# Kernel tuning notes

Measured on AMD Instinct MI355X. Metric: run time of the kernel, lower is better.

The kernel has to match this reference:

```python
import jax, jax.numpy as jnp
import numpy as np

NEG_INF = -1e9  # Keras uses a large negative for masked logits


def setup_inputs() -> dict:
    key = jax.random.key(0)
    k1, k2, k3, k4, k5 = jax.random.split(key, 5)
    B, Tq, Tv, D, U = 8, 128, 128, 512, 1024
    query = jax.random.normal(k1, (B, Tq, D), dtype=jnp.float32)
    value = jax.random.normal(k2, (B, Tv, D), dtype=jnp.float32)
    mask = jnp.ones((B, Tv), dtype=bool)
    # Dense(units, use_bias=False) kernels and AdditiveAttention scale vector
    W1 = jax.random.normal(k3, (D, U), dtype=jnp.float32) * (1.0 / np.sqrt(D))
    W2 = jax.random.normal(k4, (D, U), dtype=jnp.float32) * (1.0 / np.sqrt(D))
    scale = jax.random.normal(k5, (U,), dtype=jnp.float32) * (1.0 / np.sqrt(U))
    return {"query": query, "value": value, "mask": mask,
            "W1": W1, "W2": W2, "scale": scale}


def reference(query, value, mask, W1, W2, scale):
    # Projections (Dense, no bias)
    wq = jnp.einsum('btd,du->btu', query, W1)   # [B, Tq, U]
    wk = jnp.einsum('bsd,du->bsu', value, W2)   # [B, Tv, U]
    # Additive (Bahdanau) scores: sum_u scale_u * tanh(wq + wk)
    # Materializes [B, Tq, Tv, U] broadcast-add like Keras AdditiveAttention.
    scores = jnp.einsum('u,btsu->bts', scale,
                        jnp.tanh(wq[:, :, None, :] + wk[:, None, :, :]))
    # value mask over key axis (query_mask is all-ones in the source -> no-op)
    scores = jnp.where(mask[:, None, :], scores, NEG_INF)
    attn = jax.nn.softmax(scores, axis=-1)       # [B, Tq, Tv]
    context = jnp.einsum('bts,bsd->btd', attn, value)  # [B, Tq, D]
    return context, attn
```

## Files before the change

### kernel.cpp

```cpp
#include <hip/hip_runtime.h>

#define B_  8
#define TQ  128
#define TV  128
#define DIM 512
#define UU  1024
#define NSPLIT 8
#define NP  (B_ * TQ * TV)
#define C2  2.885390081777927f

typedef __attribute__((ext_vector_type(8))) short     short8;
typedef __attribute__((ext_vector_type(4))) float     f32x4;
typedef __attribute__((ext_vector_type(4))) unsigned short us4;

__device__ __forceinline__ unsigned short bf16_rtne(float x) {
    unsigned u = __float_as_uint(x);
    unsigned r = u + 0x7FFF + ((u >> 16) & 1);
    return (unsigned short)(r >> 16);
}
__device__ __forceinline__ float bf16_to_f(unsigned short h) {
    return __uint_as_float(((unsigned)h) << 16);
}

__global__ __launch_bounds__(256) void k_prep(
    const float* __restrict__ Q, const float* __restrict__ Vv,
    const float* __restrict__ W1, const float* __restrict__ W2,
    unsigned short* __restrict__ Ah, unsigned short* __restrict__ Al,
    unsigned short* __restrict__ Wh, unsigned short* __restrict__ Wl)
{
    __shared__ float ts[32][36];
    const int bx = blockIdx.x;
    const int t  = threadIdx.x;

    if (bx < 1024) {
        int idx = bx * 256 + t;
        int mat = idx >> 17;
        const float* src = mat ? Vv : Q;
        int off = (idx & 131071) * 4;
        float4 v = *(const float4*)&src[off];
        us4 h, l;
        h.x = bf16_rtne(v.x); l.x = bf16_rtne(v.x - bf16_to_f(h.x));
        h.y = bf16_rtne(v.y); l.y = bf16_rtne(v.y - bf16_to_f(h.y));
        h.z = bf16_rtne(v.z); l.z = bf16_rtne(v.z - bf16_to_f(h.z));
        h.w = bf16_rtne(v.w); l.w = bf16_rtne(v.w - bf16_to_f(h.w));
        *(us4*)&Ah[mat * 524288 + off] = h;
        *(us4*)&Al[mat * 524288 + off] = l;
    } else {
        int b2   = bx - 1024;
        int mat  = b2 >> 9;
        int tile = b2 & 511;
        int n0 = (tile & 31) * 32;
        int k0 = (tile >> 5) * 32;
        const float* W = mat ? W2 : W1;

        int kk = t >> 3, n4 = (t & 7) * 4;
        float4 w = *(const float4*)&W[(k0 + kk) * UU + n0 + n4];
        ts[n4 + 0][kk] = w.x; ts[n4 + 1][kk] = w.y;
        ts[n4 + 2][kk] = w.z; ts[n4 + 3][kk] = w.w;
        __syncthreads();

        int nn = t >> 3, k4 = (t & 7) * 4;
        float4 v = *(const float4*)&ts[nn][k4];
        us4 h, l;
        h.x = bf16_rtne(v.x); l.x = bf16_rtne(v.x - bf16_to_f(h.x));
        h.y = bf16_rtne(v.y); l.y = bf16_rtne(v.y - bf16_to_f(h.y));
        h.z = bf16_rtne(v.z); l.z = bf16_rtne(v.z - bf16_to_f(h.z));
        h.w = bf16_rtne(v.w); l.w = bf16_rtne(v.w - bf16_to_f(h.w));
        unsigned off = mat * 524288 + (n0 + nn) * 512 + k0 + k4;
        *(us4*)&Wh[off] = h;
        *(us4*)&Wl[off] = l;
    }
}

#define PKP 72
__global__ __launch_bounds__(256) void k_proj(
    const unsigned short* __restrict__ Ah, const unsigned short* __restrict__ Al,
    const unsigned short* __restrict__ Bh, const unsigned short* __restrict__ Bl,
    float* __restrict__ Eq, float* __restrict__ Ek)
{
    __shared__ short sAh[64 * PKP], sAl[64 * PKP], sBh[64 * PKP], sBl[64 * PKP];

    const int tid  = threadIdx.x;
    const int wave = tid >> 6;
    const int lane = tid & 63;
    const int mat  = blockIdx.z;
    const int m0   = blockIdx.y * 64;
    const int n0   = blockIdx.x * 64;

    const unsigned mb = mat * 524288u;
    const int wm = (wave & 1) * 32;
    const int wn = (wave >> 1) * 32;

    const int sm = tid >> 2, sg = tid & 3;
    const unsigned short* gAh = Ah + mb + (m0 + sm) * 512;
    const unsigned short* gAl = Al + mb + (m0 + sm) * 512;
    const unsigned short* gBh = Bh + mb + (n0 + sm) * 512;
    const unsigned short* gBl = Bl + mb + (n0 + sm) * 512;
    const int so0 = sm * PKP + sg * 8;
    const int so1 = sm * PKP + 32 + sg * 8;

    const int fr = lane & 15, fq = lane >> 4;
    const int aOff0 = (wm + fr) * PKP + fq * 8;
    const int aOff1 = (wm + 16 + fr) * PKP + fq * 8;
    const int bOff0 = (wn + fr) * PKP + fq * 8;
    const int bOff1 = (wn + 16 + fr) * PKP + fq * 8;

    f32x4 acc00 = {0.f, 0.f, 0.f, 0.f};
    f32x4 acc01 = {0.f, 0.f, 0.f, 0.f};
    f32x4 acc10 = {0.f, 0.f, 0.f, 0.f};
    f32x4 acc11 = {0.f, 0.f, 0.f, 0.f};

    int4 rAh0, rAh1, rAl0, rAl1, rBh0, rBh1, rBl0, rBl1;
    #define LOADALL(K)                                                       \
        rAh0 = *(const int4*)(gAh + (K) + sg * 8);                           \
        rAh1 = *(const int4*)(gAh + (K) + 32 + sg * 8);                      \
        rAl0 = *(const int4*)(gAl + (K) + sg * 8);                           \
        rAl1 = *(const int4*)(gAl + (K) + 32 + sg * 8);                      \
        rBh0 = *(const int4*)(gBh + (K) + sg * 8);                           \
        rBh1 = *(const int4*)(gBh + (K) + 32 + sg * 8);                      \
        rBl0 = *(const int4*)(gBl + (K) + sg * 8);                           \
        rBl1 = *(const int4*)(gBl + (K) + 32 + sg * 8);

    LOADALL(0)

    #pragma unroll 1
    for (int kc = 0; kc < 8; ++kc) {
        *(int4*)&sAh[so0] = rAh0;  *(int4*)&sAh[so1] = rAh1;
        *(int4*)&sAl[so0] = rAl0;  *(int4*)&sAl[so1] = rAl1;
        *(int4*)&sBh[so0] = rBh0;  *(int4*)&sBh[so1] = rBh1;
        *(int4*)&sBl[so0] = rBl0;  *(int4*)&sBl[so1] = rBl1;
        __syncthreads();

        if (kc < 7) { LOADALL((kc + 1) * 64) }

        #pragma unroll
        for (int ks = 0; ks < 2; ++ks) {
            const int o = ks * 32;
            short8 a0h = *(const short8*)&sAh[aOff0 + o];
            short8 a0l = *(const short8*)&sAl[aOff0 + o];
            short8 a1h = *(const short8*)&sAh[aOff1 + o];
            short8 a1l = *(const short8*)&sAl[aOff1 + o];
            short8 b0h = *(const short8*)&sBh[bOff0 + o];
            short8 b0l = *(const short8*)&sBl[bOff0 + o];
            short8 b1h = *(const short8*)&sBh[bOff1 + o];
            short8 b1l = *(const short8*)&sBl[bOff1 + o];

            acc00 = __builtin_amdgcn_mfma_f32_16x16x32_bf16(a0h, b0h, acc00, 0, 0, 0);
            acc00 = __builtin_amdgcn_mfma_f32_16x16x32_bf16(a0h, b0l, acc00, 0, 0, 0);
            acc00 = __builtin_amdgcn_mfma_f32_16x16x32_bf16(a0l, b0h, acc00, 0, 0, 0);

            acc01 = __builtin_amdgcn_mfma_f32_16x16x32_bf16(a0h, b1h, acc01, 0, 0, 0);
            acc01 = __builtin_amdgcn_mfma_f32_16x16x32_bf16(a0h, b1l, acc01, 0, 0, 0);
            acc01 = __builtin_amdgcn_mfma_f32_16x16x32_bf16(a0l, b1h, acc01, 0, 0, 0);

            acc10 = __builtin_amdgcn_mfma_f32_16x16x32_bf16(a1h, b0h, acc10, 0, 0, 0);
            acc10 = __builtin_amdgcn_mfma_f32_16x16x32_bf16(a1h, b0l, acc10, 0, 0, 0);
            acc10 = __builtin_amdgcn_mfma_f32_16x16x32_bf16(a1l, b0h, acc10, 0, 0, 0);

            acc11 = __builtin_amdgcn_mfma_f32_16x16x32_bf16(a1h, b1h, acc11, 0, 0, 0);
            acc11 = __builtin_amdgcn_mfma_f32_16x16x32_bf16(a1h, b1l, acc11, 0, 0, 0);
            acc11 = __builtin_amdgcn_mfma_f32_16x16x32_bf16(a1l, b1h, acc11, 0, 0, 0);
        }
        __syncthreads();
    }
    #undef LOADALL

    float* C = mat ? Ek : Eq;
    #pragma unroll
    for (int r = 0; r < 4; ++r) {
        int row0 = m0 + wm + fq * 4 + r;
        int row1 = row0 + 16;
        int col0 = n0 + wn + fr;
        C[row0 * UU + col0]      = __builtin_amdgcn_exp2f(C2 * acc00[r]);
        C[row0 * UU + col0 + 16] = __builtin_amdgcn_exp2f(C2 * acc01[r]);
        C[row1 * UU + col0]      = __builtin_amdgcn_exp2f(C2 * acc10[r]);
        C[row1 * UU + col0 + 16] = __builtin_amdgcn_exp2f(C2 * acc11[r]);
    }
}
#undef PKP

__global__ __launch_bounds__(256) void k_scores(
    const float* __restrict__ Eq, const float* __restrict__ Ek,
    const float* __restrict__ scale, float* __restrict__ part)
{
    __shared__ float qs[32][132];
    __shared__ float ks[32][132];
    __shared__ float ss[128];

    const int tid = threadIdx.x;
    const int tx  = tid & 15;
    const int ty  = tid >> 4;
    const int b   = blockIdx.z & 7;
    const int us  = blockIdx.z >> 3;
    const int t0  = blockIdx.y * 32;
    const int s0  = blockIdx.x * 32;
    const int u0  = us * (UU / NSPLIT);

    {
        const int c  = (tid & 31) * 4;
        const int r0 = tid >> 5;
        #pragma unroll
        for (int i = 0; i < 4; ++i) {
            int r = r0 + i * 8;
            *(float4*)&qs[r][c] = *(const float4*)&Eq[(b * TQ + t0 + r) * UU + u0 + c];
            *(float4*)&ks[r][c] = *(const float4*)&Ek[(b * TV + s0 + r) * UU + u0 + c];
        }
        if (tid < 32)
            *(float4*)&ss[tid * 4] = *(const float4*)&scale[u0 + tid * 4];
    }
    __syncthreads();

    float a00 = 0.f, a01 = 0.f, a10 = 0.f, a11 = 0.f;

    #pragma unroll 4
    for (int u4 = 0; u4 < 32; ++u4) {
        float4 q0 = *(const float4*)&qs[ty][u4 * 4];
        float4 q1 = *(const float4*)&qs[ty + 16][u4 * 4];
        float4 k0 = *(const float4*)&ks[tx][u4 * 4];
        float4 k1 = *(const float4*)&ks[tx + 16][u4 * 4];
        float4 sv = *(const float4*)&ss[u4 * 4];

        #define PAIR(ACC, QV, KV)                                           \
        {                                                                   \
            float p1 = QV.x * KV.x, p2 = QV.y * KV.y;                       \
            float b1 = p1 + 1.f,   b2 = p2 + 1.f;                           \
            float n1 = fmaf(sv.y, b1, sv.x * b2);                           \
            ACC = fmaf(n1, __builtin_amdgcn_rcpf(b1 * b2), ACC);            \
            float p3 = QV.z * KV.z, p4 = QV.w * KV.w;                       \
            float b3 = p3 + 1.f,   b4 = p4 + 1.f;                           \
            float n2 = fmaf(sv.w, b3, sv.z * b4);                           \
            ACC = fmaf(n2, __builtin_amdgcn_rcpf(b3 * b4), ACC);            \
        }
        PAIR(a00, q0, k0)
        PAIR(a01, q0, k1)
        PAIR(a10, q1, k0)
        PAIR(a11, q1, k1)
        #undef PAIR
    }

    const int t = t0 + ty, s = s0 + tx;
    float* p = &part[us * NP + (b * TQ + t) * TV + s];
    p[0]            = a00;
    p[16]           = a01;
    p[16 * TV]      = a10;
    p[16 * TV + 16] = a11;
}

__global__ __launch_bounds__(256) void k_ctx(
    const float* __restrict__ part, const int* __restrict__ mask,
    const float* __restrict__ Vv,
    float* __restrict__ attn, float* __restrict__ ctx)
{
    __shared__ float at[128][20];

    const int tid = threadIdx.x;
    const int dc  = blockIdx.x;
    const int tt  = blockIdx.y;
    const int b   = blockIdx.z;
    const int t0  = tt * 16;
    const int rg  = tid >> 4;
    const int ln  = tid & 15;
    const int base = (b * TQ + t0 + rg) * TV;

    float x[8];
    #pragma unroll
    for (int j = 0; j < 8; ++j) {
        const int s = ln + 16 * j;
        float p = 0.f;
        #pragma unroll
        for (int i = 0; i < NSPLIT; ++i) p += part[i * NP + base + s];
        x[j] = mask[b * TV + s] ? -2.f * p : -1e9f;
    }
    float m = x[0];
    #pragma unroll
    for (int j = 1; j < 8; ++j) m = fmaxf(m, x[j]);
    #pragma unroll
    for (int o = 8; o > 0; o >>= 1) m = fmaxf(m, __shfl_xor(m, o, 64));
    const float L2E = 1.4426950408889634f;
    float e[8];
    float sum = 0.f;
    #pragma unroll
    for (int j = 0; j < 8; ++j) {
        e[j] = __builtin_amdgcn_exp2f((x[j] - m) * L2E);
        sum += e[j];
    }
    #pragma unroll
    for (int o = 8; o > 0; o >>= 1) sum += __shfl_xor(sum, o, 64);
    const float r = __builtin_amdgcn_rcpf(sum);
    #pragma unroll
    for (int j = 0; j < 8; ++j) {
        const float a = e[j] * r;
        at[ln + 16 * j][rg] = a;
        if (dc == 0) attn[base + ln + 16 * j] = a;
    }
    __syncthreads();

    const int d  = (tid & 127) + dc * 128;
    const int tg = tid >> 7;
    float acc[8] = {};
    const float* vp = &Vv[b * TV * DIM + d];
    for (int s = 0; s < TV; ++s) {
        float v = vp[s * DIM];
        float4 a0 = *(const float4*)&at[s][tg * 8];
        float4 a1 = *(const float4*)&at[s][tg * 8 + 4];
        acc[0] = fmaf(a0.x, v, acc[0]);
        acc[1] = fmaf(a0.y, v, acc[1]);
        acc[2] = fmaf(a0.z, v, acc[2]);
        acc[3] = fmaf(a0.w, v, acc[3]);
        acc[4] = fmaf(a1.x, v, acc[4]);
        acc[5] = fmaf(a1.y, v, acc[5]);
        acc[6] = fmaf(a1.z, v, acc[6]);
        acc[7] = fmaf(a1.w, v, acc[7]);
    }
    #pragma unroll
    for (int j = 0; j < 8; ++j) {
        int t = t0 + tg * 8 + j;
        ctx[(b * TQ + t) * DIM + d] = acc[j];
    }
}

extern "C" void kernel_launch(void* const* d_in, const int* in_sizes, int n_in,
                              void* d_out, int out_size, void* d_ws, size_t ws_size,
                              hipStream_t stream)
{
    const float* query = (const float*)d_in[0];
    const float* value = (const float*)d_in[1];
    const int*   mask  = (const int*)d_in[2];
    const float* W1    = (const float*)d_in[3];
    const float* W2    = (const float*)d_in[4];
    const float* scale = (const float*)d_in[5];

    float* out  = (float*)d_out;
    float* ctx  = out;
    float* attn = out + B_ * TQ * DIM;

    float* Eq   = (float*)d_ws;
    float* Ek   = Eq + 1024 * 1024;
    float* part = Ek + 1024 * 1024;
    unsigned short* Ah = (unsigned short*)(part + NSPLIT * NP);
    unsigned short* Al = Ah + 2 * 1024 * 512;
    unsigned short* Wh = Al + 2 * 1024 * 512;
    unsigned short* Wl = Wh + 2 * 1024 * 512;

    hipLaunchKernelGGL(k_prep,   dim3(2048),            dim3(256), 0, stream,
                       query, value, W1, W2, Ah, Al, Wh, Wl);
    hipLaunchKernelGGL(k_proj,   dim3(16, 16, 2),       dim3(256), 0, stream,
                       Ah, Al, Wh, Wl, Eq, Ek);
    hipLaunchKernelGGL(k_scores, dim3(4, 4, 8 * NSPLIT), dim3(256), 0, stream,
                       Eq, Ek, scale, part);
    hipLaunchKernelGGL(k_ctx,    dim3(4, 8, 8),         dim3(256), 0, stream,
                       part, mask, value, attn, ctx);
}
```

Measured before the change: 112.9 us.

## Enlarge score tiles to 64x64 with 4x4 register blocking and XCD-swizzle projection blocks

The scores kernel now computes 64x64 (query, key) tiles per block with a 4x4 per-thread register tile. This cuts LDS loads per tanh-pair evaluation, and it permutes key rows in shared memory to avoid bank conflicts. The U split doubles to 16 to keep enough blocks in flight, which doubles the partial-sum buffer the context kernel must read and reduce. The projection GEMM is launched as a flat 1D grid with a block-index remap that spreads tiles across XCDs for better L2 locality.

```diff
diff --git a/kernel.cpp b/kernel.cpp
--- a/kernel.cpp
+++ b/kernel.cpp
@@ -5,7 +5,7 @@
 #define TV  128
 #define DIM 512
 #define UU  1024
-#define NSPLIT 8
+#define NSPLIT 16
 #define NP  (B_ * TQ * TV)
 #define C2  2.885390081777927f
 
@@ -83,9 +83,16 @@
     const int tid  = threadIdx.x;
     const int wave = tid >> 6;
     const int lane = tid & 63;
-    const int mat  = blockIdx.z;
-    const int m0   = blockIdx.y * 64;
-    const int n0   = blockIdx.x * 64;
+
+    const int flat = blockIdx.x;
+    const int x    = flat & 7;
+    const int j    = flat >> 3;
+    const int pair = x * 4 + (j >> 4);
+    const int nt   = pair & 15;
+    const int mat  = pair >> 4;
+    const int mt   = j & 15;
+    const int m0   = mt * 64;
+    const int n0   = nt * 64;
 
     const unsigned mb = mat * 524288u;
     const int wm = (wave & 1) * 32;
@@ -183,67 +190,69 @@
     const float* __restrict__ Eq, const float* __restrict__ Ek,
     const float* __restrict__ scale, float* __restrict__ part)
 {
-    __shared__ float qs[32][132];
-    __shared__ float ks[32][132];
-    __shared__ float ss[128];
+    __shared__ float qs[64][68];
+    __shared__ float ks[64][68];
+    __shared__ float ss[64];
 
     const int tid = threadIdx.x;
     const int tx  = tid & 15;
     const int ty  = tid >> 4;
     const int b   = blockIdx.z & 7;
     const int us  = blockIdx.z >> 3;
-    const int t0  = blockIdx.y * 32;
-    const int s0  = blockIdx.x * 32;
+    const int t0  = blockIdx.y * 64;
+    const int s0  = blockIdx.x * 64;
     const int u0  = us * (UU / NSPLIT);
 
     {
-        const int c  = (tid & 31) * 4;
-        const int r0 = tid >> 5;
+        const int r  = tid >> 2;
+        const int c0 = (tid & 3) * 16;
+        const float* srq = &Eq[(b * TQ + t0 + r) * UU + u0 + c0];
+        const float* srk = &Ek[(b * TV + s0 + r) * UU + u0 + c0];
+        const int rp = (r >> 2) | ((r & 3) << 4);
         #pragma unroll
         for (int i = 0; i < 4; ++i) {
-            int r = r0 + i * 8;
-            *(float4*)&qs[r][c] = *(const float4*)&Eq[(b * TQ + t0 + r) * UU + u0 + c];
-            *(float4*)&ks[r][c] = *(const float4*)&Ek[(b * TV + s0 + r) * UU + u0 + c];
+            *(float4*)&qs[r][c0 + i * 4]  = *(const float4*)(srq + i * 4);
+            *(float4*)&ks[rp][c0 + i * 4] = *(const float4*)(srk + i * 4);
         }
-        if (tid < 32)
+        if (tid < 16)
             *(float4*)&ss[tid * 4] = *(const float4*)&scale[u0 + tid * 4];
     }
     __syncthreads();
 
-    float a00 = 0.f, a01 = 0.f, a10 = 0.f, a11 = 0.f;
-
-    #pragma unroll 4
-    for (int u4 = 0; u4 < 32; ++u4) {
-        float4 q0 = *(const float4*)&qs[ty][u4 * 4];
-        float4 q1 = *(const float4*)&qs[ty + 16][u4 * 4];
-        float4 k0 = *(const float4*)&ks[tx][u4 * 4];
-        float4 k1 = *(const float4*)&ks[tx + 16][u4 * 4];
+    float acc[4][4] = {};
+
+    #pragma unroll 2
+    for (int u4 = 0; u4 < 16; ++u4) {
+        float4 q[4], k[4];
+        #pragma unroll
+        for (int i = 0; i < 4; ++i)
+            q[i] = *(const float4*)&qs[ty * 4 + i][u4 * 4];
+        #pragma unroll
+        for (int jj = 0; jj < 4; ++jj)
+            k[jj] = *(const float4*)&ks[tx + (jj << 4)][u4 * 4];
         float4 sv = *(const float4*)&ss[u4 * 4];
 
-        #define PAIR(ACC, QV, KV)                                           \
-        {                                                                   \
-            float p1 = QV.x * KV.x, p2 = QV.y * KV.y;                       \
-            float b1 = p1 + 1.f,   b2 = p2 + 1.f;                           \
-            float n1 = fmaf(sv.y, b1, sv.x * b2);                           \
-            ACC = fmaf(n1, __builtin_amdgcn_rcpf(b1 * b2), ACC);            \
-            float p3 = QV.z * KV.z, p4 = QV.w * KV.w;                       \
-            float b3 = p3 + 1.f,   b4 = p4 + 1.f;                           \
-            float n2 = fmaf(sv.w, b3, sv.z * b4);                           \
-            ACC = fmaf(n2, __builtin_amdgcn_rcpf(b3 * b4), ACC);            \
+        #pragma unroll
+        for (int i = 0; i < 4; ++i) {
+            #pragma unroll
+            for (int jj = 0; jj < 4; ++jj) {
+                float p1 = q[i].x * k[jj].x, p2 = q[i].y * k[jj].y;
+                float b1 = p1 + 1.f,        b2 = p2 + 1.f;
+                float n1 = fmaf(sv.y, b1, sv.x * b2);
+                acc[i][jj] = fmaf(n1, __builtin_amdgcn_rcpf(b1 * b2), acc[i][jj]);
+                float p3 = q[i].z * k[jj].z, p4 = q[i].w * k[jj].w;
+                float b3 = p3 + 1.f,        b4 = p4 + 1.f;
+                float n2 = fmaf(sv.w, b3, sv.z * b4);
+                acc[i][jj] = fmaf(n2, __builtin_amdgcn_rcpf(b3 * b4), acc[i][jj]);
+            }
         }
-        PAIR(a00, q0, k0)
-        PAIR(a01, q0, k1)
-        PAIR(a10, q1, k0)
-        PAIR(a11, q1, k1)
-        #undef PAIR
-    }
-
-    const int t = t0 + ty, s = s0 + tx;
-    float* p = &part[us * NP + (b * TQ + t) * TV + s];
-    p[0]            = a00;
-    p[16]           = a01;
-    p[16 * TV]      = a10;
-    p[16 * TV + 16] = a11;
+    }
+
+    #pragma unroll
+    for (int i = 0; i < 4; ++i) {
+        float4 o = {acc[i][0], acc[i][1], acc[i][2], acc[i][3]};
+        *(float4*)&part[us * NP + (b * TQ + t0 + ty * 4 + i) * TV + s0 + tx * 4] = o;
+    }
 }
 
 __global__ __launch_bounds__(256) void k_ctx(
@@ -342,12 +351,12 @@
     unsigned short* Wh = Al + 2 * 1024 * 512;
     unsigned short* Wl = Wh + 2 * 1024 * 512;
 
-    hipLaunchKernelGGL(k_prep,   dim3(2048),            dim3(256), 0, stream,
+    hipLaunchKernelGGL(k_prep,   dim3(2048),             dim3(256), 0, stream,
                        query, value, W1, W2, Ah, Al, Wh, Wl);
-    hipLaunchKernelGGL(k_proj,   dim3(16, 16, 2),       dim3(256), 0, stream,
+    hipLaunchKernelGGL(k_proj,   dim3(512),              dim3(256), 0, stream,
                        Ah, Al, Wh, Wl, Eq, Ek);
-    hipLaunchKernelGGL(k_scores, dim3(4, 4, 8 * NSPLIT), dim3(256), 0, stream,
+    hipLaunchKernelGGL(k_scores, dim3(2, 2, 8 * NSPLIT), dim3(256), 0, stream,
                        Eq, Ek, scale, part);
-    hipLaunchKernelGGL(k_ctx,    dim3(4, 8, 8),         dim3(256), 0, stream,
+    hipLaunchKernelGGL(k_ctx,    dim3(4, 8, 8),          dim3(256), 0, stream,
                        part, mask, value, attn, ctx);
 }
```

After: 113.7 us. About the same (+0.8%).
